# Optimization experiments

Measured on AMD Instinct MI355X. Metric: run time of the kernel, lower is better.

The kernel has to match this reference:

```python
import jax, jax.numpy as jnp
import numpy as np

N_EMBD = 1024
HEAD_SIZE = 64
B, T = 4, 4096


def setup_inputs() -> dict:
    key = jax.random.key(0)
    kx, kk, kq, kv = jax.random.split(key, 4)
    s = 1.0 / np.sqrt(N_EMBD)
    return {
        "x": jax.random.normal(kx, (B, T, N_EMBD), dtype=jnp.float32),
        "Wk": jax.random.normal(kk, (N_EMBD, HEAD_SIZE), dtype=jnp.float32) * s,
        "Wq": jax.random.normal(kq, (N_EMBD, HEAD_SIZE), dtype=jnp.float32) * s,
        "Wv": jax.random.normal(kv, (N_EMBD, HEAD_SIZE), dtype=jnp.float32) * s,
    }


def reference(x, Wk, Wq, Wv):
    Bb, Tt, C = x.shape
    k = x @ Wk  # [B,T,H]
    q = x @ Wq
    v = x @ Wv
    # scores scaled by C**-0.5 where C = n_embd (as in the original module)
    w = jnp.einsum('bth,bsh->bts', q, k) * (C ** -0.5)  # [B,T,T]
    causal = jnp.tril(jnp.ones((Tt, Tt), dtype=bool))
    w = jnp.where(causal, w, -jnp.inf)
    w = jax.nn.softmax(w, axis=-1)
    # dropout prob is 0.0 (eval) -> identity
    out = jnp.einsum('bts,bsh->bth', w, v)  # [B,T,H]
    return out
```

## Files before the change

### kernel.cpp

```cpp
#include <hip/hip_runtime.h>


#define BSZ 4
#define TSZ 4096
#define CSZ 1024
#define MSZ (BSZ * TSZ)
#define NS 8
#define QT 128
#define NQT (TSZ / QT)

typedef _Float16 half8 __attribute__((ext_vector_type(8)));
typedef _Float16 half4 __attribute__((ext_vector_type(4)));
typedef float f32x4 __attribute__((ext_vector_type(4)));

#define MFMA(a, b, c) __builtin_amdgcn_mfma_f32_16x16x32_f16((a), (b), (c), 0, 0, 0)
#define QSCALE 0.04508422002778011f

__global__ __launch_bounds__(256) void wconv(const float* __restrict__ Wk,
                                             const float* __restrict__ Wq,
                                             const float* __restrict__ Wv,
                                             _Float16* __restrict__ Wt) {
    int idx = blockIdx.x * 256 + threadIdx.x;
    int n = idx >> 10;
    int kk = idx & 1023;
    const float* W = (n < 64) ? Wk : ((n < 128) ? Wq : Wv);
    float v = W[kk * 64 + (n & 63)];
    if (n >= 64 && n < 128) v *= QSCALE;
    Wt[idx] = (_Float16)v;
}

__global__ __launch_bounds__(256) void qkv_proj(const float* __restrict__ x,
                                                const _Float16* __restrict__ Wt,
                                                _Float16* __restrict__ kbf,
                                                _Float16* __restrict__ qbf,
                                                _Float16* __restrict__ vbf) {
    __shared__ _Float16 xt[32 * 64];

    int tid = threadIdx.x;
    int wave = tid >> 6, lane = tid & 63;
    int quad = lane >> 4, l16 = lane & 15;
    int row0 = blockIdx.x * 32;

    f32x4 acc[6];
#pragma unroll
    for (int i = 0; i < 6; i++) acc[i] = (f32x4){0.f, 0.f, 0.f, 0.f};

    int sr = tid >> 3;
    int sc = tid & 7;
    const float* xrow = x + (size_t)(row0 + sr) * CSZ + sc * 8;

    f32x4 p0 = *(const f32x4*)xrow;
    f32x4 p1 = *(const f32x4*)(xrow + 4);

    for (int kc = 0; kc < CSZ; kc += 64) {
        __syncthreads();
        {
            _Float16 tmp[8] __attribute__((aligned(16)));
#pragma unroll
            for (int i = 0; i < 4; i++) {
                tmp[i] = (_Float16)p0[i];
                tmp[4 + i] = (_Float16)p1[i];
            }
            *(half8*)&xt[sr * 64 + (sc ^ (sr & 7)) * 8] = *(half8*)tmp;
        }
        __syncthreads();
        if (kc + 64 < CSZ) {
            p0 = *(const f32x4*)(xrow + kc + 64);
            p1 = *(const f32x4*)(xrow + kc + 68);
        }
#pragma unroll
        for (int s = 0; s < 2; s++) {
            half8 a0 = *(half8*)&xt[l16 * 64 + ((s * 4 + quad) ^ (l16 & 7)) * 8];
            half8 a1 = *(half8*)&xt[(16 + l16) * 64 +
                                    ((s * 4 + quad) ^ (l16 & 7)) * 8];
#pragma unroll
            for (int j = 0; j < 3; j++) {
                int ct = wave * 3 + j;
                half8 bb = *(const half8*)&Wt[(size_t)(ct * 16 + l16) * CSZ +
                                              kc + s * 32 + quad * 8];
                acc[j * 2 + 0] = MFMA(a0, bb, acc[j * 2 + 0]);
                acc[j * 2 + 1] = MFMA(a1, bb, acc[j * 2 + 1]);
            }
        }
    }

    _Float16* outs[3] = {kbf, qbf, vbf};
#pragma unroll
    for (int j = 0; j < 3; j++) {
        int ct = wave * 3 + j;
        _Float16* o = outs[ct >> 2];
        int col = (ct & 3) * 16 + l16;
#pragma unroll
        for (int m = 0; m < 2; m++) {
#pragma unroll
            for (int r = 0; r < 4; r++) {
                int row = row0 + m * 16 + quad * 4 + r;
                o[(size_t)row * 64 + col] = (_Float16)acc[j * 2 + m][r];
            }
        }
    }
}

__global__ __launch_bounds__(256) void vtrans(const _Float16* __restrict__ vbf,
                                              _Float16* __restrict__ vtb) {
    __shared__ _Float16 tile[64 * 72];
    int tid = threadIdx.x;
    int b = blockIdx.x >> 6, g = blockIdx.x & 63;
    int r = tid >> 2, cg = tid & 3;
    const _Float16* src = vbf + ((size_t)b * TSZ + g * 64 + r) * 64;
    *(half8*)&tile[r * 72 + cg * 16] = *(const half8*)&src[cg * 16];
    *(half8*)&tile[r * 72 + cg * 16 + 8] = *(const half8*)&src[cg * 16 + 8];
    __syncthreads();
    int h = tid >> 2, seg = tid & 3;
    _Float16* dst = vtb + ((size_t)b * 64 + h) * TSZ + g * 64;
#pragma unroll
    for (int i = 0; i < 16; i++) {
        int t_off = seg * 16 + i;
        int p = (t_off & 15) * 4 + (t_off >> 4);
        dst[p] = tile[t_off * 72 + h];
    }
}

__global__ __launch_bounds__(256) void attn_partial(
    const _Float16* __restrict__ qbf, const _Float16* __restrict__ kbf,
    const _Float16* __restrict__ vtb, _Float16* __restrict__ opart,
    float* __restrict__ ml) {
    __shared__ _Float16 kt[64 * 64];
    __shared__ _Float16 vt[64 * 64];
    __shared__ _Float16 pt[QT * 64];

    int tid = threadIdx.x;
    int wave = tid >> 6, lane = tid & 63;
    int quad = lane >> 4, l16 = lane & 15;
    int s = blockIdx.x & (NS - 1);
    int qt = (blockIdx.x >> 3) & (NQT - 1);
    int b = blockIdx.x >> 8;
    int nt = 2 * (qt + 1);
    int lo = s * nt / NS, hi = (s + 1) * nt / NS;
    int part = (b * NQT + qt) * NS + s;

    if (lo >= hi) {
        if (tid < QT) ml[part * QT + tid] = 0.f;
        return;
    }

    const _Float16* qb = qbf + (size_t)b * TSZ * 64;
    const _Float16* kb = kbf + (size_t)b * TSZ * 64;
    const _Float16* vb = vtb + (size_t)b * 64 * TSZ;

    int qrow = qt * QT + wave * 32;
    half8 aq[2][2];
#pragma unroll
    for (int st = 0; st < 2; st++)
#pragma unroll
        for (int ss = 0; ss < 2; ss++)
            aq[st][ss] = *(const half8*)&qb[(qrow + st * 16 + l16) * 64 +
                                            ss * 32 + quad * 8];

    f32x4 o[2][4];
    float l_acc[2][4];
#pragma unroll
    for (int st = 0; st < 2; st++)
#pragma unroll
        for (int ct = 0; ct < 4; ct++) {
            o[st][ct] = (f32x4){0.f, 0.f, 0.f, 0.f};
            l_acc[st][ct] = 0.f;
        }

    int sr = tid >> 2;
    int scc = (tid & 3) * 2;
    half8 pk0, pk1, pv0, pv1;
    {
        const _Float16* ks = kb + ((size_t)(lo * 64 + sr)) * 64 + scc * 8;
        pk0 = *(const half8*)ks;
        pk1 = *(const half8*)(ks + 8);
        const _Float16* vs = vb + (size_t)sr * TSZ + lo * 64 + scc * 8;
        pv0 = *(const half8*)vs;
        pv1 = *(const half8*)(vs + 8);
    }

    for (int kti = lo; kti < hi; kti++) {
        __syncthreads();
        *(half8*)&kt[sr * 64 + (scc ^ (sr & 7)) * 8] = pk0;
        *(half8*)&kt[sr * 64 + ((scc + 1) ^ (sr & 7)) * 8] = pk1;
        *(half8*)&vt[sr * 64 + (scc ^ (sr & 7)) * 8] = pv0;
        *(half8*)&vt[sr * 64 + ((scc + 1) ^ (sr & 7)) * 8] = pv1;
        __syncthreads();
        if (kti + 1 < hi) {
            const _Float16* ks = kb + ((size_t)((kti + 1) * 64 + sr)) * 64 + scc * 8;
            pk0 = *(const half8*)ks;
            pk1 = *(const half8*)(ks + 8);
            const _Float16* vs = vb + (size_t)sr * TSZ + (kti + 1) * 64 + scc * 8;
            pv0 = *(const half8*)vs;
            pv1 = *(const half8*)(vs + 8);
        }

        f32x4 sacc[2][4];
#pragma unroll
        for (int st = 0; st < 2; st++)
#pragma unroll
            for (int ct = 0; ct < 4; ct++)
                sacc[st][ct] = (f32x4){0.f, 0.f, 0.f, 0.f};
#pragma unroll
        for (int ss = 0; ss < 2; ss++) {
#pragma unroll
            for (int ct = 0; ct < 4; ct++) {
                half8 bb = *(half8*)&kt[(ct * 16 + l16) * 64 +
                                        ((ss * 4 + quad) ^ (l16 & 7)) * 8];
                sacc[0][ct] = MFMA(aq[0][ss], bb, sacc[0][ct]);
                sacc[1][ct] = MFMA(aq[1][ss], bb, sacc[1][ct]);
            }
        }

        bool diag = (kti >= 2 * qt);
#pragma unroll
        for (int st = 0; st < 2; st++) {
#pragma unroll
            for (int r = 0; r < 4; r++) {
                int lrow = wave * 32 + st * 16 + quad * 4 + r;
                float pv[4];
#pragma unroll
                for (int ct = 0; ct < 4; ct++) {
                    float e = exp2f(sacc[st][ct][r]);
                    if (diag) {
                        int key = kti * 64 + ct * 16 + l16;
                        int rowg = qt * QT + lrow;
                        if (key > rowg) e = 0.f;
                    }
                    pv[ct] = e;
                }
                l_acc[st][r] += pv[0] + pv[1] + pv[2] + pv[3];
                half4 hp;
#pragma unroll
                for (int ct = 0; ct < 4; ct++) hp[ct] = (_Float16)pv[ct];
                int chunk = (l16 >> 1) ^ (lrow & 7);
                *(half4*)&pt[lrow * 64 + chunk * 8 + (l16 & 1) * 4] = hp;
            }
        }

#pragma unroll
        for (int ss = 0; ss < 2; ss++) {
            half8 ap0 = *(half8*)&pt[(wave * 32 + l16) * 64 +
                                     ((ss * 4 + quad) ^ (l16 & 7)) * 8];
            half8 ap1 = *(half8*)&pt[(wave * 32 + 16 + l16) * 64 +
                                     ((ss * 4 + quad) ^ (l16 & 7)) * 8];
#pragma unroll
            for (int ct = 0; ct < 4; ct++) {
                half8 bv = *(half8*)&vt[(ct * 16 + l16) * 64 +
                                        ((ss * 4 + quad) ^ (l16 & 7)) * 8];
                o[0][ct] = MFMA(ap0, bv, o[0][ct]);
                o[1][ct] = MFMA(ap1, bv, o[1][ct]);
            }
        }
    }

#pragma unroll
    for (int off = 1; off < 16; off <<= 1) {
#pragma unroll
        for (int st = 0; st < 2; st++)
#pragma unroll
            for (int r = 0; r < 4; r++)
                l_acc[st][r] += __shfl_xor(l_acc[st][r], off);
    }

    _Float16* op = opart + (size_t)part * (QT * 64);
#pragma unroll
    for (int st = 0; st < 2; st++) {
#pragma unroll
        for (int r = 0; r < 4; r++) {
            int lrow = wave * 32 + st * 16 + quad * 4 + r;
            float li = l_acc[st][r];
            float inv = li > 0.f ? 1.f / li : 0.f;
#pragma unroll
            for (int ct = 0; ct < 4; ct++)
                op[lrow * 64 + ct * 16 + l16] = (_Float16)(o[st][ct][r] * inv);
            if (l16 == 0) ml[part * QT + lrow] = li;
        }
    }
}

__global__ __launch_bounds__(256) void combine(
    const _Float16* __restrict__ opart, const float* __restrict__ ml,
    float* __restrict__ out) {
    int tid = threadIdx.x;
    int row = blockIdx.x * 64 + (tid >> 2);
    int seg = (tid & 3) * 16;
    int b = row >> 12;
    int qt = (row >> 7) & (NQT - 1);
    int prow = row & (QT - 1);
    int pbase = (b * NQT + qt) * NS;

    float acc[16];
#pragma unroll
    for (int i = 0; i < 16; i++) acc[i] = 0.f;
    float lsum = 0.f;
#pragma unroll
    for (int s = 0; s < NS; s++) {
        float l = ml[(pbase + s) * QT + prow];
        lsum += l;
        const _Float16* op =
            opart + (size_t)(pbase + s) * (QT * 64) + prow * 64 + seg;
        half8 h0 = *(const half8*)op;
        half8 h1 = *(const half8*)(op + 8);
#pragma unroll
        for (int i = 0; i < 8; i++) {
            acc[i] += l * (float)h0[i];
            acc[8 + i] += l * (float)h1[i];
        }
    }
    float inv = 1.f / lsum;
    float* ob = out + (size_t)row * 64 + seg;
#pragma unroll
    for (int i = 0; i < 16; i++) ob[i] = acc[i] * inv;
}

extern "C" void kernel_launch(void* const* d_in, const int* in_sizes, int n_in,
                              void* d_out, int out_size, void* d_ws,
                              size_t ws_size, hipStream_t stream) {
    (void)in_sizes; (void)n_in; (void)out_size; (void)ws_size;
    const float* x = (const float*)d_in[0];
    const float* Wk = (const float*)d_in[1];
    const float* Wq = (const float*)d_in[2];
    const float* Wv = (const float*)d_in[3];

    _Float16* Wt = (_Float16*)d_ws;
    _Float16* kbf = Wt + 192 * 1024;
    _Float16* qbf = kbf + (size_t)MSZ * 64;
    _Float16* vbf = qbf + (size_t)MSZ * 64;
    _Float16* vtb = vbf + (size_t)MSZ * 64;
    _Float16* opart = vtb + (size_t)MSZ * 64;
    float* ml = (float*)(opart + (size_t)BSZ * NQT * NS * QT * 64);

    wconv<<<768, 256, 0, stream>>>(Wk, Wq, Wv, Wt);
    qkv_proj<<<MSZ / 32, 256, 0, stream>>>(x, Wt, kbf, qbf, vbf);
    vtrans<<<BSZ * 64, 256, 0, stream>>>(vbf, vtb);
    attn_partial<<<BSZ * NQT * NS, 256, 0, stream>>>(qbf, kbf, vtb, opart, ml);
    combine<<<MSZ / 64, 256, 0, stream>>>(opart, ml, (float*)d_out);
}
```

Measured before the change: 161.5 us.

## Pre-swizzle K/V tiles in projection, drop vtrans, async LDS double-buffer attention

The projection kernel now writes K and transposed V straight into tile-blocked, pre-swizzled images that match the attention kernel's LDS layout. This removes the separate V transpose kernel and one intermediate buffer. The attention loop double-buffers K/V tiles and fills them with global_load_lds direct-to-LDS copies instead of register staging plus LDS stores, dropping one barrier per tile. The projection kernel also uses a 128-wide double-buffered K chunk, wconv is reindexed for coalesced reads, and combine uses finer-grained threads. The scattered per-element stores of the swizzled K/V images may be less coalesced, and the extra LDS buffers raise shared memory per block.

```diff
diff --git a/kernel.cpp b/kernel.cpp
--- a/kernel.cpp
+++ b/kernel.cpp
@@ -16,25 +16,38 @@
 #define MFMA(a, b, c) __builtin_amdgcn_mfma_f32_16x16x32_f16((a), (b), (c), 0, 0, 0)
 #define QSCALE 0.04508422002778011f
 
-__global__ __launch_bounds__(256) void wconv(const float* __restrict__ Wk,
+__device__ __forceinline__ int kimg(int r, int h) {
+    return r * 64 + ((((h >> 3) ^ (r & 7))) << 3) + (h & 7);
+}
+__device__ __forceinline__ int vimg(int kk, int h) {
+    int p = (kk & 15) * 4 + (kk >> 4);
+    return h * 64 + ((((p >> 3) ^ (h & 7))) << 3) + (p & 7);
+}
+
+__device__ __forceinline__ void glds16(const _Float16* g, _Float16* l) {
+    __builtin_amdgcn_global_load_lds(
+        (const __attribute__((address_space(1))) void*)g,
+        (__attribute__((address_space(3))) void*)l, 16, 0, 0);
+}
+
+__global__ __launch_bounds__(192) void wconv(const float* __restrict__ Wk,
                                              const float* __restrict__ Wq,
                                              const float* __restrict__ Wv,
                                              _Float16* __restrict__ Wt) {
-    int idx = blockIdx.x * 256 + threadIdx.x;
-    int n = idx >> 10;
-    int kk = idx & 1023;
+    int kk = blockIdx.x;
+    int n = threadIdx.x;
     const float* W = (n < 64) ? Wk : ((n < 128) ? Wq : Wv);
     float v = W[kk * 64 + (n & 63)];
     if (n >= 64 && n < 128) v *= QSCALE;
-    Wt[idx] = (_Float16)v;
+    Wt[(size_t)n * 1024 + kk] = (_Float16)v;
 }
 
 __global__ __launch_bounds__(256) void qkv_proj(const float* __restrict__ x,
                                                 const _Float16* __restrict__ Wt,
-                                                _Float16* __restrict__ kbf,
                                                 _Float16* __restrict__ qbf,
-                                                _Float16* __restrict__ vbf) {
-    __shared__ _Float16 xt[32 * 64];
+                                                _Float16* __restrict__ kbs,
+                                                _Float16* __restrict__ vts) {
+    __shared__ _Float16 xt[2][32 * 128];
 
     int tid = threadIdx.x;
     int wave = tid >> 6, lane = tid & 63;
@@ -47,86 +60,75 @@
 
     int sr = tid >> 3;
     int sc = tid & 7;
-    const float* xrow = x + (size_t)(row0 + sr) * CSZ + sc * 8;
-
-    f32x4 p0 = *(const f32x4*)xrow;
-    f32x4 p1 = *(const f32x4*)(xrow + 4);
-
-    for (int kc = 0; kc < CSZ; kc += 64) {
+    const float* xrow = x + (size_t)(row0 + sr) * CSZ + sc * 16;
+
+    f32x4 p[4];
+#pragma unroll
+    for (int i = 0; i < 4; i++) p[i] = *(const f32x4*)(xrow + i * 4);
+
+    int cur = 0;
+    for (int kc = 0; kc < CSZ; kc += 128, cur ^= 1) {
+        {
+            _Float16 tmp[16] __attribute__((aligned(16)));
+#pragma unroll
+            for (int i = 0; i < 16; i++) tmp[i] = (_Float16)p[i >> 2][i & 3];
+            *(half8*)&xt[cur][sr * 128 + ((sc * 2) ^ (sr & 7)) * 8] =
+                *(half8*)tmp;
+            *(half8*)&xt[cur][sr * 128 + ((sc * 2 + 1) ^ (sr & 7)) * 8] =
+                *(half8*)(tmp + 8);
+        }
         __syncthreads();
-        {
-            _Float16 tmp[8] __attribute__((aligned(16)));
-#pragma unroll
-            for (int i = 0; i < 4; i++) {
-                tmp[i] = (_Float16)p0[i];
-                tmp[4 + i] = (_Float16)p1[i];
-            }
-            *(half8*)&xt[sr * 64 + (sc ^ (sr & 7)) * 8] = *(half8*)tmp;
-        }
-        __syncthreads();
-        if (kc + 64 < CSZ) {
-            p0 = *(const f32x4*)(xrow + kc + 64);
-            p1 = *(const f32x4*)(xrow + kc + 68);
-        }
-#pragma unroll
-        for (int s = 0; s < 2; s++) {
-            half8 a0 = *(half8*)&xt[l16 * 64 + ((s * 4 + quad) ^ (l16 & 7)) * 8];
-            half8 a1 = *(half8*)&xt[(16 + l16) * 64 +
-                                    ((s * 4 + quad) ^ (l16 & 7)) * 8];
+        if (kc + 128 < CSZ) {
+#pragma unroll
+            for (int i = 0; i < 4; i++)
+                p[i] = *(const f32x4*)(xrow + kc + 128 + i * 4);
+        }
+#pragma unroll
+        for (int ss = 0; ss < 4; ss++) {
+            half8 a0 = *(half8*)&xt[cur][l16 * 128 +
+                                         ((ss * 4 + quad) ^ (l16 & 7)) * 8];
+            half8 a1 = *(half8*)&xt[cur][(16 + l16) * 128 +
+                                         ((ss * 4 + quad) ^ (l16 & 7)) * 8];
 #pragma unroll
             for (int j = 0; j < 3; j++) {
                 int ct = wave * 3 + j;
                 half8 bb = *(const half8*)&Wt[(size_t)(ct * 16 + l16) * CSZ +
-                                              kc + s * 32 + quad * 8];
+                                              kc + ss * 32 + quad * 8];
                 acc[j * 2 + 0] = MFMA(a0, bb, acc[j * 2 + 0]);
                 acc[j * 2 + 1] = MFMA(a1, bb, acc[j * 2 + 1]);
             }
         }
     }
 
-    _Float16* outs[3] = {kbf, qbf, vbf};
 #pragma unroll
     for (int j = 0; j < 3; j++) {
         int ct = wave * 3 + j;
-        _Float16* o = outs[ct >> 2];
+        int kind = ct >> 2;
         int col = (ct & 3) * 16 + l16;
 #pragma unroll
         for (int m = 0; m < 2; m++) {
 #pragma unroll
             for (int r = 0; r < 4; r++) {
                 int row = row0 + m * 16 + quad * 4 + r;
-                o[(size_t)row * 64 + col] = (_Float16)acc[j * 2 + m][r];
-            }
-        }
-    }
-}
-
-__global__ __launch_bounds__(256) void vtrans(const _Float16* __restrict__ vbf,
-                                              _Float16* __restrict__ vtb) {
-    __shared__ _Float16 tile[64 * 72];
-    int tid = threadIdx.x;
-    int b = blockIdx.x >> 6, g = blockIdx.x & 63;
-    int r = tid >> 2, cg = tid & 3;
-    const _Float16* src = vbf + ((size_t)b * TSZ + g * 64 + r) * 64;
-    *(half8*)&tile[r * 72 + cg * 16] = *(const half8*)&src[cg * 16];
-    *(half8*)&tile[r * 72 + cg * 16 + 8] = *(const half8*)&src[cg * 16 + 8];
-    __syncthreads();
-    int h = tid >> 2, seg = tid & 3;
-    _Float16* dst = vtb + ((size_t)b * 64 + h) * TSZ + g * 64;
-#pragma unroll
-    for (int i = 0; i < 16; i++) {
-        int t_off = seg * 16 + i;
-        int p = (t_off & 15) * 4 + (t_off >> 4);
-        dst[p] = tile[t_off * 72 + h];
+                _Float16 val = (_Float16)acc[j * 2 + m][r];
+                if (kind == 0) {
+                    kbs[((size_t)(row >> 6)) * 4096 + kimg(row & 63, col)] = val;
+                } else if (kind == 1) {
+                    qbf[(size_t)row * 64 + col] = val;
+                } else {
+                    vts[((size_t)(row >> 6)) * 4096 + vimg(row & 63, col)] = val;
+                }
+            }
+        }
     }
 }
 
 __global__ __launch_bounds__(256) void attn_partial(
-    const _Float16* __restrict__ qbf, const _Float16* __restrict__ kbf,
-    const _Float16* __restrict__ vtb, _Float16* __restrict__ opart,
+    const _Float16* __restrict__ qbf, const _Float16* __restrict__ kbs,
+    const _Float16* __restrict__ vts, _Float16* __restrict__ opart,
     float* __restrict__ ml) {
-    __shared__ _Float16 kt[64 * 64];
-    __shared__ _Float16 vt[64 * 64];
+    __shared__ _Float16 kt[2][4096];
+    __shared__ _Float16 vt[2][4096];
     __shared__ _Float16 pt[QT * 64];
 
     int tid = threadIdx.x;
@@ -145,8 +147,8 @@
     }
 
     const _Float16* qb = qbf + (size_t)b * TSZ * 64;
-    const _Float16* kb = kbf + (size_t)b * TSZ * 64;
-    const _Float16* vb = vtb + (size_t)b * 64 * TSZ;
+    const _Float16* kbs_b = kbs + (size_t)b * 64 * 4096;
+    const _Float16* vts_b = vts + (size_t)b * 64 * 4096;
 
     int qrow = qt * QT + wave * 32;
     half8 aq[2][2];
@@ -167,32 +169,27 @@
             l_acc[st][ct] = 0.f;
         }
 
-    int sr = tid >> 2;
-    int scc = (tid & 3) * 2;
-    half8 pk0, pk1, pv0, pv1;
+    int soff = wave * 512 + lane * 8;
+
     {
-        const _Float16* ks = kb + ((size_t)(lo * 64 + sr)) * 64 + scc * 8;
-        pk0 = *(const half8*)ks;
-        pk1 = *(const half8*)(ks + 8);
-        const _Float16* vs = vb + (size_t)sr * TSZ + lo * 64 + scc * 8;
-        pv0 = *(const half8*)vs;
-        pv1 = *(const half8*)(vs + 8);
-    }
-
-    for (int kti = lo; kti < hi; kti++) {
-        __syncthreads();
-        *(half8*)&kt[sr * 64 + (scc ^ (sr & 7)) * 8] = pk0;
-        *(half8*)&kt[sr * 64 + ((scc + 1) ^ (sr & 7)) * 8] = pk1;
-        *(half8*)&vt[sr * 64 + (scc ^ (sr & 7)) * 8] = pv0;
-        *(half8*)&vt[sr * 64 + ((scc + 1) ^ (sr & 7)) * 8] = pv1;
+        const _Float16* ks = kbs_b + (size_t)lo * 4096 + soff;
+        const _Float16* vs = vts_b + (size_t)lo * 4096 + soff;
+        glds16(ks, &kt[0][soff]);
+        glds16(ks + 2048, &kt[0][2048 + soff]);
+        glds16(vs, &vt[0][soff]);
+        glds16(vs + 2048, &vt[0][2048 + soff]);
+    }
+
+    int cur = 0;
+    for (int kti = lo; kti < hi; kti++, cur ^= 1) {
         __syncthreads();
         if (kti + 1 < hi) {
-            const _Float16* ks = kb + ((size_t)((kti + 1) * 64 + sr)) * 64 + scc * 8;
-            pk0 = *(const half8*)ks;
-            pk1 = *(const half8*)(ks + 8);
-            const _Float16* vs = vb + (size_t)sr * TSZ + (kti + 1) * 64 + scc * 8;
-            pv0 = *(const half8*)vs;
-            pv1 = *(const half8*)(vs + 8);
+            const _Float16* ks = kbs_b + (size_t)(kti + 1) * 4096 + soff;
+            const _Float16* vs = vts_b + (size_t)(kti + 1) * 4096 + soff;
+            glds16(ks, &kt[cur ^ 1][soff]);
+            glds16(ks + 2048, &kt[cur ^ 1][2048 + soff]);
+            glds16(vs, &vt[cur ^ 1][soff]);
+            glds16(vs + 2048, &vt[cur ^ 1][2048 + soff]);
         }
 
         f32x4 sacc[2][4];
@@ -205,8 +202,8 @@
         for (int ss = 0; ss < 2; ss++) {
 #pragma unroll
             for (int ct = 0; ct < 4; ct++) {
-                half8 bb = *(half8*)&kt[(ct * 16 + l16) * 64 +
-                                        ((ss * 4 + quad) ^ (l16 & 7)) * 8];
+                half8 bb = *(half8*)&kt[cur][(ct * 16 + l16) * 64 +
+                                             ((ss * 4 + quad) ^ (l16 & 7)) * 8];
                 sacc[0][ct] = MFMA(aq[0][ss], bb, sacc[0][ct]);
                 sacc[1][ct] = MFMA(aq[1][ss], bb, sacc[1][ct]);
             }
@@ -224,8 +221,7 @@
                     float e = exp2f(sacc[st][ct][r]);
                     if (diag) {
                         int key = kti * 64 + ct * 16 + l16;
-                        int rowg = qt * QT + lrow;
-                        if (key > rowg) e = 0.f;
+                        if (key > qt * QT + lrow) e = 0.f;
                     }
                     pv[ct] = e;
                 }
@@ -246,8 +242,8 @@
                                      ((ss * 4 + quad) ^ (l16 & 7)) * 8];
 #pragma unroll
             for (int ct = 0; ct < 4; ct++) {
-                half8 bv = *(half8*)&vt[(ct * 16 + l16) * 64 +
-                                        ((ss * 4 + quad) ^ (l16 & 7)) * 8];
+                half8 bv = *(half8*)&vt[cur][(ct * 16 + l16) * 64 +
+                                             ((ss * 4 + quad) ^ (l16 & 7)) * 8];
                 o[0][ct] = MFMA(ap0, bv, o[0][ct]);
                 o[1][ct] = MFMA(ap1, bv, o[1][ct]);
             }
@@ -283,35 +279,30 @@
     const _Float16* __restrict__ opart, const float* __restrict__ ml,
     float* __restrict__ out) {
     int tid = threadIdx.x;
-    int row = blockIdx.x * 64 + (tid >> 2);
-    int seg = (tid & 3) * 16;
+    int row = blockIdx.x * 32 + (tid >> 3);
+    int seg = (tid & 7) * 8;
     int b = row >> 12;
     int qt = (row >> 7) & (NQT - 1);
     int prow = row & (QT - 1);
     int pbase = (b * NQT + qt) * NS;
 
-    float acc[16];
-#pragma unroll
-    for (int i = 0; i < 16; i++) acc[i] = 0.f;
+    float acc[8];
+#pragma unroll
+    for (int i = 0; i < 8; i++) acc[i] = 0.f;
     float lsum = 0.f;
 #pragma unroll
     for (int s = 0; s < NS; s++) {
         float l = ml[(pbase + s) * QT + prow];
         lsum += l;
-        const _Float16* op =
-            opart + (size_t)(pbase + s) * (QT * 64) + prow * 64 + seg;
-        half8 h0 = *(const half8*)op;
-        half8 h1 = *(const half8*)(op + 8);
-#pragma unroll
-        for (int i = 0; i < 8; i++) {
-            acc[i] += l * (float)h0[i];
-            acc[8 + i] += l * (float)h1[i];
-        }
+        half8 h = *(const half8*)&opart[(size_t)(pbase + s) * (QT * 64) +
+                                        prow * 64 + seg];
+#pragma unroll
+        for (int i = 0; i < 8; i++) acc[i] += l * (float)h[i];
     }
     float inv = 1.f / lsum;
     float* ob = out + (size_t)row * 64 + seg;
 #pragma unroll
-    for (int i = 0; i < 16; i++) ob[i] = acc[i] * inv;
+    for (int i = 0; i < 8; i++) ob[i] = acc[i] * inv;
 }
 
 extern "C" void kernel_launch(void* const* d_in, const int* in_sizes, int n_in,
@@ -324,16 +315,14 @@
     const float* Wv = (const float*)d_in[3];
 
     _Float16* Wt = (_Float16*)d_ws;
-    _Float16* kbf = Wt + 192 * 1024;
-    _Float16* qbf = kbf + (size_t)MSZ * 64;
-    _Float16* vbf = qbf + (size_t)MSZ * 64;
-    _Float16* vtb = vbf + (size_t)MSZ * 64;
-    _Float16* opart = vtb + (size_t)MSZ * 64;
+    _Float16* qbf = Wt + 192 * 1024;
+    _Float16* kbs = qbf + (size_t)MSZ * 64;
+    _Float16* vts = kbs + (size_t)MSZ * 64;
+    _Float16* opart = vts + (size_t)MSZ * 64;
     float* ml = (float*)(opart + (size_t)BSZ * NQT * NS * QT * 64);
 
-    wconv<<<768, 256, 0, stream>>>(Wk, Wq, Wv, Wt);
-    qkv_proj<<<MSZ / 32, 256, 0, stream>>>(x, Wt, kbf, qbf, vbf);
-    vtrans<<<BSZ * 64, 256, 0, stream>>>(vbf, vtb);
-    attn_partial<<<BSZ * NQT * NS, 256, 0, stream>>>(qbf, kbf, vtb, opart, ml);
-    combine<<<MSZ / 64, 256, 0, stream>>>(opart, ml, (float*)d_out);
-}
+    wconv<<<1024, 192, 0, stream>>>(Wk, Wq, Wv, Wt);
+    qkv_proj<<<MSZ / 32, 256, 0, stream>>>(x, Wt, qbf, kbs, vts);
+    attn_partial<<<BSZ * NQT * NS, 256, 0, stream>>>(qbf, kbs, vts, opart, ml);
+    combine<<<MSZ / 32, 256, 0, stream>>>(opart, ml, (float*)d_out);
+}
```

Result: no change. 162.3 us (+0.5%).
